# Performance work log

Hardware: AMD Instinct MI355X
Metric: run time of the kernel (lower is better)

The kernel has to match this reference:

```python
import jax, jax.numpy as jnp
import numpy as np

D = 768      # d_model == d_patch (16*16*3)
DFF = 3072
NH = 12
DH = D // NH  # 64
P = 16
IMG = 224
HP = IMG // P  # 14
NP = HP * HP   # 196
L = NP + 1     # 197 with CLS
NL = 12        # layers (weights SHARED across layers, per original code)
NC = 1000


def _pos_enc(length, d):
    # Faithful to PositionalEncoding: even dims sin with exponent i, odd dims cos with exponent i-1
    pos = jnp.arange(length, dtype=jnp.float32)[:, None]          # [L,1]
    dim = jnp.arange(d)
    i = jnp.where(dim % 2 == 0, dim, (dim // 2) * 2).astype(jnp.float32)
    ang = pos / jnp.power(10000.0, i / d)                          # [L,D]
    return jnp.where(dim % 2 == 0, jnp.sin(ang), jnp.cos(ang))


def _ln(x, g, b, eps=1e-5):
    m = x.mean(-1, keepdims=True)
    v = x.var(-1, keepdims=True)
    return (x - m) / jnp.sqrt(v + eps) * g + b


def setup_inputs() -> dict:
    key = jax.random.key(0)
    ks = jax.random.split(key, 12)
    s = 0.02
    n = lambda k, shp: jax.random.normal(k, shp, jnp.float32) * s
    return {
        "x": jax.random.normal(ks[0], (32, 3, IMG, IMG), jnp.float32),
        "w_proj": n(ks[1], (D, D)), "b_proj": jnp.zeros((D,), jnp.float32),
        "cls_emb": jnp.zeros((1, 1, D), jnp.float32),
        "ln1_g": jnp.ones((D,), jnp.float32), "ln1_b": jnp.zeros((D,), jnp.float32),
        "w_qkv": n(ks[2], (3 * D, D)), "b_qkv": jnp.zeros((3 * D,), jnp.float32),
        "w_o": n(ks[3], (D, D)), "b_o": jnp.zeros((D,), jnp.float32),
        "ln2_g": jnp.ones((D,), jnp.float32), "ln2_b": jnp.zeros((D,), jnp.float32),
        "w_fc1": n(ks[4], (DFF, D)), "b_fc1": jnp.zeros((DFF,), jnp.float32),
        "w_fc2": n(ks[5], (D, DFF)), "b_fc2": jnp.zeros((D,), jnp.float32),
        "lnf_g": jnp.ones((D,), jnp.float32), "lnf_b": jnp.zeros((D,), jnp.float32),
        "w_h": n(ks[6], (D, D)), "b_h": jnp.zeros((D,), jnp.float32),
        "w_c": n(ks[7], (NC, D)), "b_c": jnp.zeros((NC,), jnp.float32),
    }


def reference(x, w_proj, b_proj, cls_emb, ln1_g, ln1_b, w_qkv, b_qkv, w_o, b_o,
              ln2_g, ln2_b, w_fc1, b_fc1, w_fc2, b_fc2, lnf_g, lnf_b,
              w_h, b_h, w_c, b_c):
    b = x.shape[0]
    # convert_to_patch: unfold -> channel-major patch features [b, NP, 3*P*P]
    patches = x.reshape(b, 3, HP, P, HP, P).transpose(0, 2, 4, 1, 3, 5).reshape(b, NP, 3 * P * P)
    emb = patches @ w_proj.T + b_proj                              # [b,NP,D]
    cls = jnp.broadcast_to(cls_emb, (b, 1, D))
    h = jnp.concatenate([cls, emb], axis=1) + _pos_enc(L, D)[None]  # [b,L,D]

    inv_sqrt_dk = 1.0 / jnp.sqrt(jnp.float32(DH))
    for _ in range(NL):  # SAME weights every layer (faithful to nn.Sequential of one object)
        y = _ln(h, ln1_g, ln1_b)
        qkv = y @ w_qkv.T + b_qkv                                   # [b,L,3D]
        # faithful non-standard head split: view(b,l,3*DH,NH).transpose -> [b,NH,L,3*DH]
        qkv = qkv.reshape(b, L, 3 * DH, NH).transpose(0, 3, 1, 2)
        q, k, v = jnp.split(qkv, 3, axis=-1)                        # each [b,NH,L,DH]
        attn = jax.nn.softmax(jnp.einsum('bhld,bhmd->bhlm', q, k) * inv_sqrt_dk, axis=-1)
        o = jnp.einsum('bhlm,bhmd->bhld', attn, v)                  # [b,NH,L,DH]
        o = o.transpose(0, 2, 1, 3).reshape(b, L, D)
        h = h + (o @ w_o.T + b_o)
        y = _ln(h, ln2_g, ln2_b)
        f = jax.nn.gelu(y @ w_fc1.T + b_fc1, approximate=False) @ w_fc2.T + b_fc2
        h = h + f

    rep = _ln(h[:, 0], lnf_g, lnf_b)                                # [b,D]
    hid = jnp.tanh(rep @ w_h.T + b_h)                               # is_pretrain=True
    return hid @ w_c.T + b_c                                        # [b,NC]
```

## Files before the change

kernel.cpp:

```cpp
#include <hip/hip_runtime.h>
#include <hip/hip_bf16.h>


typedef __bf16 bf16;
typedef __bf16 bf16x8 __attribute__((ext_vector_type(8)));
typedef __bf16 bf16x4 __attribute__((ext_vector_type(4)));
typedef float  f32x4  __attribute__((ext_vector_type(4)));

typedef __attribute__((address_space(1))) const unsigned int gu32;
typedef __attribute__((address_space(3))) unsigned int lu32;

static __device__ __forceinline__ f32x4 mfma_bf16(bf16x8 a, bf16x8 b, f32x4 c) {
  return __builtin_amdgcn_mfma_f32_16x16x32_bf16(a, b, c, 0, 0, 0);
}
static __device__ __forceinline__ void gll16(const bf16* g, bf16* l) {
  __builtin_amdgcn_global_load_lds((gu32*)g, (lu32*)l, 16, 0, 0);
}


__global__ __launch_bounds__(256) void f2b_k(const float* __restrict__ a, bf16* __restrict__ o, int n) {
  int i = blockIdx.x * 256 + threadIdx.x;
  if (i < n) o[i] = (bf16)a[i];
}

__global__ __launch_bounds__(256) void posenc_k(float* __restrict__ pos) {
  int l = blockIdx.x;
  for (int d = threadIdx.x; d < 768; d += 256) {
    int ieff = d & ~1;
    float ang = (float)l * expf(-(float)ieff * (9.210340371976184f / 768.0f));
    pos[l * 768 + d] = (d & 1) ? cosf(ang) : sinf(ang);
  }
}

__global__ __launch_bounds__(256) void patchify_k(const float* __restrict__ x, bf16* __restrict__ p) {
  int idx = blockIdx.x * 256 + threadIdx.x;
  int t = idx / 768, col = idx - t * 768;
  int b = t / 196, pp = t - b * 196;
  int ph = pp / 14, pw = pp - ph * 14;
  int c = col >> 8, r = col & 255, i = r >> 4, j = r & 15;
  p[idx] = (bf16)x[((b * 3 + c) * 224 + ph * 16 + i) * 224 + pw * 16 + j];
}

__global__ __launch_bounds__(256) void combine_k(float* __restrict__ h, const float* __restrict__ pos,
                                                 const float* __restrict__ cls) {
  int idx = blockIdx.x * 256 + threadIdx.x;
  int t = idx / 768, d = idx - t * 768;
  int l = t % 197;
  float p = pos[l * 768 + d];
  if (l == 0) h[idx] = cls[d] + p;
  else        h[idx] += p;
}

template<int PAD>
__global__ __launch_bounds__(256) void ln4_k(const float* __restrict__ x, const float* __restrict__ g,
                                             const float* __restrict__ bb, bf16* __restrict__ y,
                                             int nrows, int instride) {
  const int wave = threadIdx.x >> 6, lane = threadIdx.x & 63;
  const int row = blockIdx.x * 4 + wave;
  if (row >= nrows) return;
  const float4* x4 = (const float4*)(x + (size_t)row * instride);
  float4 v0 = x4[lane], v1 = x4[lane + 64], v2 = x4[lane + 128];
  float s  = v0.x + v0.y + v0.z + v0.w + v1.x + v1.y + v1.z + v1.w + v2.x + v2.y + v2.z + v2.w;
  float s2 = v0.x*v0.x + v0.y*v0.y + v0.z*v0.z + v0.w*v0.w
           + v1.x*v1.x + v1.y*v1.y + v1.z*v1.z + v1.w*v1.w
           + v2.x*v2.x + v2.y*v2.y + v2.z*v2.z + v2.w*v2.w;
  #pragma unroll
  for (int o = 1; o < 64; o <<= 1) { s += __shfl_xor(s, o); s2 += __shfl_xor(s2, o); }
  float m = s * (1.0f / 768.0f);
  float inv = rsqrtf(s2 * (1.0f / 768.0f) - m * m + 1e-5f);
  int orow = row;
  if (PAD) { int bq = row / 197; orow = row + bq * 3; }
  bf16* yr = y + (size_t)orow * 768;
  const float4* g4 = (const float4*)g;
  const float4* b4 = (const float4*)bb;
  #pragma unroll
  for (int i = 0; i < 3; ++i) {
    int idx = lane + i * 64;
    float4 vv = (i == 0) ? v0 : (i == 1) ? v1 : v2;
    float4 gv = g4[idx], bv = b4[idx];
    bf16x4 o;
    o[0] = (bf16)((vv.x - m) * inv * gv.x + bv.x);
    o[1] = (bf16)((vv.y - m) * inv * gv.y + bv.y);
    o[2] = (bf16)((vv.z - m) * inv * gv.z + bv.z);
    o[3] = (bf16)((vv.w - m) * inv * gv.w + bv.w);
    *(bf16x4*)(yr + idx * 4) = o;
  }
}

template<int BN, int EPI>
__global__ __launch_bounds__(256) void gemm2(
    const bf16* __restrict__ A, const bf16* __restrict__ B,
    int M, int N, int K, int ldc, const float* __restrict__ bias,
    float* __restrict__ outF, bf16* __restrict__ outB)
{
  constexpr int WN = (BN == 128) ? 64 : 32;
  constexpr int NI = WN / 16;
  constexpr int NB = BN / 32;
  __shared__ alignas(16) bf16 As[2][128 * 64];
  __shared__ alignas(16) bf16 Bs[2][BN * 64];
  const int tid = threadIdx.x;
  const int lane = tid & 63, wave = tid >> 6;
  const int wr = wave >> 1, wc = wave & 1;
  const int lrow = lane & 15, lgrp = lane >> 4;
  const int row0 = blockIdx.x * 128, col0 = blockIdx.y * BN;

  f32x4 acc[4][NI] = {};
  const bf16* Agb = A + (size_t)row0 * K;
  const bf16* Bgb = B + (size_t)col0 * K;
  const int srow = lane >> 3, schunk = lane & 7;
  const int nk = K >> 6;

  #pragma unroll
  for (int i = 0; i < 4; ++i) {
    int rr = (wave * 4 + i) * 8 + srow;
    int g = schunk ^ (rr & 7);
    gll16(Agb + (size_t)rr * K + g * 8, As[0] + (wave * 4 + i) * 512);
  }
  #pragma unroll
  for (int i = 0; i < NB; ++i) {
    int rr = (wave * NB + i) * 8 + srow;
    int g = schunk ^ (rr & 7);
    gll16(Bgb + (size_t)rr * K + g * 8, Bs[0] + (wave * NB + i) * 512);
  }
  __syncthreads();

  int cur = 0;
  for (int kt = 0; kt < nk; ++kt) {
    if (kt + 1 < nk) {
      const bf16* Ag = Agb + (kt + 1) * 64;
      const bf16* Bg = Bgb + (kt + 1) * 64;
      bf16* Ad = As[cur ^ 1]; bf16* Bd = Bs[cur ^ 1];
      #pragma unroll
      for (int i = 0; i < 4; ++i) {
        int rr = (wave * 4 + i) * 8 + srow;
        int g = schunk ^ (rr & 7);
        gll16(Ag + (size_t)rr * K + g * 8, Ad + (wave * 4 + i) * 512);
      }
      #pragma unroll
      for (int i = 0; i < NB; ++i) {
        int rr = (wave * NB + i) * 8 + srow;
        int g = schunk ^ (rr & 7);
        gll16(Bg + (size_t)rr * K + g * 8, Bd + (wave * NB + i) * 512);
      }
    }
    const bf16* Ac = As[cur]; const bf16* Bc = Bs[cur];
    #pragma unroll
    for (int kk = 0; kk < 2; ++kk) {
      bf16x8 af[4], bfr[NI];
      #pragma unroll
      for (int mi = 0; mi < 4; ++mi) {
        int r = wr * 64 + mi * 16 + lrow;
        af[mi] = *(const bf16x8*)(Ac + r * 64 + (((kk * 4 + lgrp) ^ (r & 7)) << 3));
      }
      #pragma unroll
      for (int ni = 0; ni < NI; ++ni) {
        int r = wc * WN + ni * 16 + lrow;
        bfr[ni] = *(const bf16x8*)(Bc + r * 64 + (((kk * 4 + lgrp) ^ (r & 7)) << 3));
      }
      __builtin_amdgcn_s_setprio(1);
      #pragma unroll
      for (int mi = 0; mi < 4; ++mi)
        #pragma unroll
        for (int ni = 0; ni < NI; ++ni)
          acc[mi][ni] = mfma_bf16(af[mi], bfr[ni], acc[mi][ni]);
      __builtin_amdgcn_s_setprio(0);
    }
    __syncthreads();
    cur ^= 1;
  }

  #pragma unroll
  for (int ni = 0; ni < NI; ++ni) {
    const int col = col0 + wc * WN + ni * 16 + lrow;
    float bs = 0.0f;
    if (EPI != 1) {
      if (EPI == 5) bs = (col < N) ? bias[col] : 0.0f;
      else          bs = bias[col];
    }
    #pragma unroll
    for (int mi = 0; mi < 4; ++mi) {
      const int rbase = row0 + wr * 64 + mi * 16 + (lgrp << 2);
      #pragma unroll
      for (int j = 0; j < 4; ++j) {
        const int t = rbase + j;
        if (EPI == 1) {
          float val = acc[mi][ni][j] + bias[t];
          if (t < 768) val *= 0.125f;
          outB[(size_t)t * ldc + col] = (bf16)val;
        } else {
          if (t >= M) continue;
          float val = acc[mi][ni][j] + bs;
          if (EPI == 0) {
            int b = t / 196, p = t - b * 196;
            outF[((size_t)(b * 197 + 1 + p)) * 768 + col] = val;
          } else if (EPI == 2) {
            outF[(size_t)t * 768 + col] += val;
          } else if (EPI == 3) {
            outB[(size_t)t * 3072 + col] = (bf16)(0.5f * val * (1.0f + erff(val * 0.70710678118654752f)));
          } else if (EPI == 4) {
            outB[(size_t)t * 768 + col] = (bf16)tanhf(val);
          } else {
            if (col < N) outF[(size_t)t * ldc + col] = val;
          }
        }
      }
    }
  }
}

__global__ __launch_bounds__(512) void attn_k(const bf16* __restrict__ Ct, bf16* __restrict__ O) {
  __shared__ alignas(16) bf16 Ks[208 * 64];
  __shared__ alignas(16) bf16 Qs[208 * 64];
  __shared__ alignas(16) bf16 Vs[64 * 232];
  __shared__ alignas(16) bf16 Ps[8][16 * 232];
  const int bh = blockIdx.x;
  const int b = bh / 12, hh = bh - b * 12;
  const int tid = threadIdx.x, lane = tid & 63, wave = tid >> 6;
  const int lrow = lane & 15, lgrp = lane >> 4;
  const size_t tc0 = (size_t)b * 200;

  for (int task = tid; task < 1600; task += 512) {
    int d = task / 25, lc = task - d * 25;
    int l0 = lc * 8;
    const size_t cb = tc0 + l0;
    bf16x8 qv = *(const bf16x8*)(Ct + ((size_t)(d * 12 + hh)) * 6400 + cb);
    bf16x8 kv = *(const bf16x8*)(Ct + ((size_t)(768 + d * 12 + hh)) * 6400 + cb);
    bf16x8 vv = *(const bf16x8*)(Ct + ((size_t)(1536 + d * 12 + hh)) * 6400 + cb);
    #pragma unroll
    for (int e = 0; e < 8; ++e) {
      int l = l0 + e;
      int sw = ((((d >> 3) ^ (l & 7)) << 3) | (d & 7));
      Ks[l * 64 + sw] = kv[e];
      Qs[l * 64 + sw] = qv[e];
    }
    *(bf16x8*)(Vs + d * 232 + l0) = vv;
  }
  for (int q = tid; q < 64 * 35; q += 512) {
    int d = q / 35, c = 197 + (q - d * 35);
    Vs[d * 232 + c] = (bf16)0.0f;
  }
  __syncthreads();

  for (int rt = wave; rt < 13; rt += 8) {
    const int r = rt * 16 + lrow;
    bf16x8 a0 = *(const bf16x8*)(Qs + r * 64 + ((lgrp ^ (r & 7)) << 3));
    bf16x8 a1 = *(const bf16x8*)(Qs + r * 64 + (((4 + lgrp) ^ (r & 7)) << 3));
    f32x4 sacc[13];
    #pragma unroll
    for (int ct = 0; ct < 13; ++ct) {
      const int kr = ct * 16 + lrow;
      bf16x8 b0 = *(const bf16x8*)(Ks + kr * 64 + ((lgrp ^ (kr & 7)) << 3));
      bf16x8 b1 = *(const bf16x8*)(Ks + kr * 64 + (((4 + lgrp) ^ (kr & 7)) << 3));
      f32x4 s = {};
      s = mfma_bf16(a0, b0, s);
      s = mfma_bf16(a1, b1, s);
      sacc[ct] = s;
    }
    bf16* Pw = Ps[wave];
    float inv4[4];
    #pragma unroll
    for (int j = 0; j < 4; ++j) {
      const int prow = (lgrp << 2) + j;
      float mx = -3.0e38f;
      #pragma unroll
      for (int ct = 0; ct < 13; ++ct) {
        int c = ct * 16 + lrow;
        if (c < 197) mx = fmaxf(mx, sacc[ct][j]);
      }
      #pragma unroll
      for (int o = 1; o < 16; o <<= 1) mx = fmaxf(mx, __shfl_xor(mx, o));
      float sum = 0.0f;
      #pragma unroll
      for (int ct = 0; ct < 13; ++ct) {
        int c = ct * 16 + lrow;
        float p = (c < 197) ? __expf(sacc[ct][j] - mx) : 0.0f;
        sum += p;
        Pw[prow * 232 + c] = (bf16)p;
      }
      #pragma unroll
      for (int o = 1; o < 16; o <<= 1) sum += __shfl_xor(sum, o);
      inv4[j] = 1.0f / sum;
      Pw[prow * 232 + 208 + lrow] = (bf16)0.0f;
    }
    f32x4 oacc[4] = {};
    #pragma unroll
    for (int mc = 0; mc < 7; ++mc) {
      bf16x8 pa = *(const bf16x8*)(Pw + lrow * 232 + mc * 32 + (lgrp << 3));
      #pragma unroll
      for (int n2 = 0; n2 < 4; ++n2) {
        bf16x8 vb = *(const bf16x8*)(Vs + (n2 * 16 + lrow) * 232 + mc * 32 + (lgrp << 3));
        oacc[n2] = mfma_bf16(pa, vb, oacc[n2]);
      }
    }
    #pragma unroll
    for (int n2 = 0; n2 < 4; ++n2) {
      const int d = n2 * 16 + lrow;
      #pragma unroll
      for (int j = 0; j < 4; ++j) {
        const int qrow = rt * 16 + (lgrp << 2) + j;
        if (qrow < 197)
          O[((size_t)b * 197 + qrow) * 768 + hh * 64 + d] = (bf16)(oacc[n2][j] * inv4[j]);
      }
    }
  }
}


extern "C" void kernel_launch(void* const* d_in, const int* in_sizes, int n_in,
                              void* d_out, int out_size, void* d_ws, size_t ws_size,
                              hipStream_t stream) {
  const float* x      = (const float*)d_in[0];
  const float* w_proj = (const float*)d_in[1];
  const float* b_proj = (const float*)d_in[2];
  const float* cls    = (const float*)d_in[3];
  const float* ln1g   = (const float*)d_in[4];
  const float* ln1b   = (const float*)d_in[5];
  const float* w_qkv  = (const float*)d_in[6];
  const float* b_qkv  = (const float*)d_in[7];
  const float* w_o    = (const float*)d_in[8];
  const float* b_o    = (const float*)d_in[9];
  const float* ln2g   = (const float*)d_in[10];
  const float* ln2b   = (const float*)d_in[11];
  const float* w_fc1  = (const float*)d_in[12];
  const float* b_fc1  = (const float*)d_in[13];
  const float* w_fc2  = (const float*)d_in[14];
  const float* b_fc2  = (const float*)d_in[15];
  const float* lnfg   = (const float*)d_in[16];
  const float* lnfb   = (const float*)d_in[17];
  const float* w_h    = (const float*)d_in[18];
  const float* b_h    = (const float*)d_in[19];
  const float* w_c    = (const float*)d_in[20];
  const float* b_c    = (const float*)d_in[21];
  float* out = (float*)d_out;

  uint8_t* ws = (uint8_t*)d_ws;
  size_t off = 0;
  auto alloc = [&](size_t bytes) -> void* {
    void* p = ws + off; off += (bytes + 255) & ~(size_t)255; return p;
  };
  float* h    = (float*)alloc(6400ull * 768 * 4);
  bf16*  ybf  = (bf16*) alloc(6400ull * 768 * 2);
  bf16*  ct   = (bf16*) alloc(2304ull * 6400 * 2);
  bf16*  ob   = (bf16*) alloc(6400ull * 768 * 2);
  bf16*  f1   = (bf16*) alloc(6400ull * 3072 * 2);
  float* pos  = (float*)alloc(197ull * 768 * 4);
  bf16* wprojB = (bf16*)alloc(768ull * 768 * 2);
  bf16* wqkvB  = (bf16*)alloc(2304ull * 768 * 2);
  bf16* woB    = (bf16*)alloc(768ull * 768 * 2);
  bf16* wfc1B  = (bf16*)alloc(3072ull * 768 * 2);
  bf16* wfc2B  = (bf16*)alloc(768ull * 3072 * 2);
  bf16* whB    = (bf16*)alloc(768ull * 768 * 2);
  bf16* wcB    = (bf16*)alloc(1024ull * 768 * 2);
  bf16* repB   = (bf16*)alloc(128ull * 768 * 2);
  bf16* hidB   = (bf16*)alloc(128ull * 768 * 2);
  bf16* patches = f1;

  f2b_k<<<(768 * 768 + 255) / 256, 256, 0, stream>>>(w_proj, wprojB, 768 * 768);
  f2b_k<<<(2304 * 768 + 255) / 256, 256, 0, stream>>>(w_qkv, wqkvB, 2304 * 768);
  f2b_k<<<(768 * 768 + 255) / 256, 256, 0, stream>>>(w_o, woB, 768 * 768);
  f2b_k<<<(3072 * 768 + 255) / 256, 256, 0, stream>>>(w_fc1, wfc1B, 3072 * 768);
  f2b_k<<<(768 * 3072 + 255) / 256, 256, 0, stream>>>(w_fc2, wfc2B, 768 * 3072);
  f2b_k<<<(768 * 768 + 255) / 256, 256, 0, stream>>>(w_h, whB, 768 * 768);
  f2b_k<<<(1000 * 768 + 255) / 256, 256, 0, stream>>>(w_c, wcB, 1000 * 768);
  posenc_k<<<197, 256, 0, stream>>>(pos);
  patchify_k<<<6272 * 768 / 256, 256, 0, stream>>>(x, patches);
  gemm2<64, 0><<<dim3(49, 12), 256, 0, stream>>>(patches, wprojB, 6272, 768, 768, 768, b_proj, h, nullptr);
  combine_k<<<6304 * 768 / 256, 256, 0, stream>>>(h, pos, cls);

  for (int layer = 0; layer < 12; ++layer) {
    ln4_k<1><<<1576, 256, 0, stream>>>(h, ln1g, ln1b, ybf, 6304, 768);
    gemm2<128, 1><<<dim3(18, 50), 256, 0, stream>>>(wqkvB, ybf, 2304, 6400, 768, 6400, b_qkv, nullptr, ct);
    attn_k<<<384, 512, 0, stream>>>(ct, ob);
    gemm2<64, 2><<<dim3(50, 12), 256, 0, stream>>>(ob, woB, 6304, 768, 768, 768, b_o, h, nullptr);
    ln4_k<0><<<1576, 256, 0, stream>>>(h, ln2g, ln2b, ybf, 6304, 768);
    gemm2<128, 3><<<dim3(50, 24), 256, 0, stream>>>(ybf, wfc1B, 6304, 3072, 768, 3072, b_fc1, nullptr, f1);
    gemm2<64, 2><<<dim3(50, 12), 256, 0, stream>>>(f1, wfc2B, 6304, 768, 3072, 768, b_fc2, h, nullptr);
  }

  ln4_k<0><<<8, 256, 0, stream>>>(h, lnfg, lnfb, repB, 32, 197 * 768);
  gemm2<64, 4><<<dim3(1, 12), 256, 0, stream>>>(repB, whB, 32, 768, 768, 768, b_h, nullptr, hidB);
  gemm2<64, 5><<<dim3(1, 16), 256, 0, stream>>>(hidB, wcB, 32, 1000, 768, 1000, b_c, out, nullptr);
}
```

Measured before the change: 2.962 ms.

## Remap GEMM blocks per XCD, single-buffer big tiles, fuse posenc into projection

The GEMM grid becomes 1D, and the block index is remapped so that consecutive tiles land on the same XCD, which should improve L2 reuse of the shared A/B panels on the multi-die GPU. The large-tile GEMMs (QKV, FC1) switch to a single LDS buffer with a sync-load-compute-sync loop, cutting LDS use to raise occupancy at the cost of losing load/compute overlap. The positional-encoding add moves into the patch-projection epilogue, and a tiny kernel writes only the CLS rows, removing a full-tensor pass.

Result: no change. 2.954 ms (-0.3%).

```diff
diff --git a/kernel.cpp b/kernel.cpp
--- a/kernel.cpp
+++ b/kernel.cpp
@@ -41,14 +41,11 @@
   p[idx] = (bf16)x[((b * 3 + c) * 224 + ph * 16 + i) * 224 + pw * 16 + j];
 }
 
-__global__ __launch_bounds__(256) void combine_k(float* __restrict__ h, const float* __restrict__ pos,
-                                                 const float* __restrict__ cls) {
-  int idx = blockIdx.x * 256 + threadIdx.x;
-  int t = idx / 768, d = idx - t * 768;
-  int l = t % 197;
-  float p = pos[l * 768 + d];
-  if (l == 0) h[idx] = cls[d] + p;
-  else        h[idx] += p;
+__global__ __launch_bounds__(256) void cls_k(float* __restrict__ h, const float* __restrict__ pos,
+                                             const float* __restrict__ cls) {
+  int b = blockIdx.x;
+  for (int d = threadIdx.x; d < 768; d += 256)
+    h[((size_t)b * 197) * 768 + d] = cls[d] + pos[d];
 }
 
 template<int PAD>
@@ -87,22 +84,30 @@
   }
 }
 
-template<int BN, int EPI>
+template<int BN, int EPI, bool DBUF>
 __global__ __launch_bounds__(256) void gemm2(
     const bf16* __restrict__ A, const bf16* __restrict__ B,
-    int M, int N, int K, int ldc, const float* __restrict__ bias,
+    int M, int N, int K, int ldc, int gx, const float* __restrict__ bias,
+    const float* __restrict__ posw,
     float* __restrict__ outF, bf16* __restrict__ outB)
 {
   constexpr int WN = (BN == 128) ? 64 : 32;
   constexpr int NI = WN / 16;
   constexpr int NB = BN / 32;
-  __shared__ alignas(16) bf16 As[2][128 * 64];
-  __shared__ alignas(16) bf16 Bs[2][BN * 64];
+  constexpr int NBUF = DBUF ? 2 : 1;
+  __shared__ alignas(16) bf16 As[NBUF][128 * 64];
+  __shared__ alignas(16) bf16 Bs[NBUF][BN * 64];
   const int tid = threadIdx.x;
   const int lane = tid & 63, wave = tid >> 6;
   const int wr = wave >> 1, wc = wave & 1;
   const int lrow = lane & 15, lgrp = lane >> 4;
-  const int row0 = blockIdx.x * 128, col0 = blockIdx.y * BN;
+
+  const int nwg = gridDim.x, bid0 = blockIdx.x;
+  const int xcd = bid0 & 7, loc = bid0 >> 3;
+  const int q = nwg >> 3, r = nwg & 7;
+  const int nb = (xcd < r ? xcd * (q + 1) : r * (q + 1) + (xcd - r) * q) + loc;
+  const int bx = nb % gx, by = nb / gx;
+  const int row0 = bx * 128, col0 = by * BN;
 
   f32x4 acc[4][NI] = {};
   const bf16* Agb = A + (size_t)row0 * K;
@@ -110,52 +115,35 @@
   const int srow = lane >> 3, schunk = lane & 7;
   const int nk = K >> 6;
 
-  #pragma unroll
-  for (int i = 0; i < 4; ++i) {
-    int rr = (wave * 4 + i) * 8 + srow;
-    int g = schunk ^ (rr & 7);
-    gll16(Agb + (size_t)rr * K + g * 8, As[0] + (wave * 4 + i) * 512);
-  }
-  #pragma unroll
-  for (int i = 0; i < NB; ++i) {
-    int rr = (wave * NB + i) * 8 + srow;
-    int g = schunk ^ (rr & 7);
-    gll16(Bgb + (size_t)rr * K + g * 8, Bs[0] + (wave * NB + i) * 512);
-  }
-  __syncthreads();
-
-  int cur = 0;
-  for (int kt = 0; kt < nk; ++kt) {
-    if (kt + 1 < nk) {
-      const bf16* Ag = Agb + (kt + 1) * 64;
-      const bf16* Bg = Bgb + (kt + 1) * 64;
-      bf16* Ad = As[cur ^ 1]; bf16* Bd = Bs[cur ^ 1];
-      #pragma unroll
-      for (int i = 0; i < 4; ++i) {
-        int rr = (wave * 4 + i) * 8 + srow;
-        int g = schunk ^ (rr & 7);
-        gll16(Ag + (size_t)rr * K + g * 8, Ad + (wave * 4 + i) * 512);
-      }
-      #pragma unroll
-      for (int i = 0; i < NB; ++i) {
-        int rr = (wave * NB + i) * 8 + srow;
-        int g = schunk ^ (rr & 7);
-        gll16(Bg + (size_t)rr * K + g * 8, Bd + (wave * NB + i) * 512);
-      }
-    }
-    const bf16* Ac = As[cur]; const bf16* Bc = Bs[cur];
+  auto stageA = [&](const bf16* Ag, bf16* Ad) {
+    #pragma unroll
+    for (int i = 0; i < 4; ++i) {
+      int rr = (wave * 4 + i) * 8 + srow;
+      int g = schunk ^ (rr & 7);
+      gll16(Ag + (size_t)rr * K + g * 8, Ad + (wave * 4 + i) * 512);
+    }
+  };
+  auto stageB = [&](const bf16* Bg, bf16* Bd) {
+    #pragma unroll
+    for (int i = 0; i < NB; ++i) {
+      int rr = (wave * NB + i) * 8 + srow;
+      int g = schunk ^ (rr & 7);
+      gll16(Bg + (size_t)rr * K + g * 8, Bd + (wave * NB + i) * 512);
+    }
+  };
+  auto compute = [&](const bf16* Ac, const bf16* Bc) {
     #pragma unroll
     for (int kk = 0; kk < 2; ++kk) {
       bf16x8 af[4], bfr[NI];
       #pragma unroll
       for (int mi = 0; mi < 4; ++mi) {
-        int r = wr * 64 + mi * 16 + lrow;
-        af[mi] = *(const bf16x8*)(Ac + r * 64 + (((kk * 4 + lgrp) ^ (r & 7)) << 3));
+        int rrr = wr * 64 + mi * 16 + lrow;
+        af[mi] = *(const bf16x8*)(Ac + rrr * 64 + (((kk * 4 + lgrp) ^ (rrr & 7)) << 3));
       }
       #pragma unroll
       for (int ni = 0; ni < NI; ++ni) {
-        int r = wc * WN + ni * 16 + lrow;
-        bfr[ni] = *(const bf16x8*)(Bc + r * 64 + (((kk * 4 + lgrp) ^ (r & 7)) << 3));
+        int rrr = wc * WN + ni * 16 + lrow;
+        bfr[ni] = *(const bf16x8*)(Bc + rrr * 64 + (((kk * 4 + lgrp) ^ (rrr & 7)) << 3));
       }
       __builtin_amdgcn_s_setprio(1);
       #pragma unroll
@@ -165,8 +153,28 @@
           acc[mi][ni] = mfma_bf16(af[mi], bfr[ni], acc[mi][ni]);
       __builtin_amdgcn_s_setprio(0);
     }
+  };
+
+  if constexpr (DBUF) {
+    stageA(Agb, As[0]); stageB(Bgb, Bs[0]);
     __syncthreads();
-    cur ^= 1;
+    int cur = 0;
+    for (int kt = 0; kt < nk; ++kt) {
+      if (kt + 1 < nk) {
+        stageA(Agb + (kt + 1) * 64, As[cur ^ 1]);
+        stageB(Bgb + (kt + 1) * 64, Bs[cur ^ 1]);
+      }
+      compute(As[cur], Bs[cur]);
+      __syncthreads();
+      cur ^= 1;
+    }
+  } else {
+    for (int kt = 0; kt < nk; ++kt) {
+      stageA(Agb + kt * 64, As[0]); stageB(Bgb + kt * 64, Bs[0]);
+      __syncthreads();
+      compute(As[0], Bs[0]);
+      __syncthreads();
+    }
   }
 
   #pragma unroll
@@ -192,7 +200,7 @@
           float val = acc[mi][ni][j] + bs;
           if (EPI == 0) {
             int b = t / 196, p = t - b * 196;
-            outF[((size_t)(b * 197 + 1 + p)) * 768 + col] = val;
+            outF[((size_t)(b * 197 + 1 + p)) * 768 + col] = val + posw[(size_t)(1 + p) * 768 + col];
           } else if (EPI == 2) {
             outF[(size_t)t * 768 + col] += val;
           } else if (EPI == 3) {
@@ -364,20 +372,27 @@
   f2b_k<<<(1000 * 768 + 255) / 256, 256, 0, stream>>>(w_c, wcB, 1000 * 768);
   posenc_k<<<197, 256, 0, stream>>>(pos);
   patchify_k<<<6272 * 768 / 256, 256, 0, stream>>>(x, patches);
-  gemm2<64, 0><<<dim3(49, 12), 256, 0, stream>>>(patches, wprojB, 6272, 768, 768, 768, b_proj, h, nullptr);
-  combine_k<<<6304 * 768 / 256, 256, 0, stream>>>(h, pos, cls);
+  gemm2<64, 0, true><<<49 * 12, 256, 0, stream>>>(patches, wprojB, 6272, 768, 768, 768, 49,
+                                                  b_proj, pos, h, nullptr);
+  cls_k<<<32, 256, 0, stream>>>(h, pos, cls);
 
   for (int layer = 0; layer < 12; ++layer) {
     ln4_k<1><<<1576, 256, 0, stream>>>(h, ln1g, ln1b, ybf, 6304, 768);
-    gemm2<128, 1><<<dim3(18, 50), 256, 0, stream>>>(wqkvB, ybf, 2304, 6400, 768, 6400, b_qkv, nullptr, ct);
+    gemm2<128, 1, false><<<18 * 50, 256, 0, stream>>>(wqkvB, ybf, 2304, 6400, 768, 6400, 18,
+                                                      b_qkv, nullptr, nullptr, ct);
     attn_k<<<384, 512, 0, stream>>>(ct, ob);
-    gemm2<64, 2><<<dim3(50, 12), 256, 0, stream>>>(ob, woB, 6304, 768, 768, 768, b_o, h, nullptr);
+    gemm2<64, 2, true><<<50 * 12, 256, 0, stream>>>(ob, woB, 6304, 768, 768, 768, 50,
+                                                    b_o, nullptr, h, nullptr);
     ln4_k<0><<<1576, 256, 0, stream>>>(h, ln2g, ln2b, ybf, 6304, 768);
-    gemm2<128, 3><<<dim3(50, 24), 256, 0, stream>>>(ybf, wfc1B, 6304, 3072, 768, 3072, b_fc1, nullptr, f1);
-    gemm2<64, 2><<<dim3(50, 12), 256, 0, stream>>>(f1, wfc2B, 6304, 768, 3072, 768, b_fc2, h, nullptr);
+    gemm2<128, 3, false><<<50 * 24, 256, 0, stream>>>(ybf, wfc1B, 6304, 3072, 768, 3072, 50,
+                                                      b_fc1, nullptr, nullptr, f1);
+    gemm2<64, 2, true><<<50 * 12, 256, 0, stream>>>(f1, wfc2B, 6304, 768, 3072, 768, 50,
+                                                    b_fc2, nullptr, h, nullptr);
   }
 
   ln4_k<0><<<8, 256, 0, stream>>>(h, lnfg, lnfb, repB, 32, 197 * 768);
-  gemm2<64, 4><<<dim3(1, 12), 256, 0, stream>>>(repB, whB, 32, 768, 768, 768, b_h, nullptr, hidB);
-  gemm2<64, 5><<<dim3(1, 16), 256, 0, stream>>>(hidB, wcB, 32, 1000, 768, 1000, b_c, out, nullptr);
-}
+  gemm2<64, 4, true><<<1 * 12, 256, 0, stream>>>(repB, whB, 32, 768, 768, 768, 1,
+                                                 b_h, nullptr, nullptr, hidB);
+  gemm2<64, 5, true><<<1 * 16, 256, 0, stream>>>(hidB, wcB, 32, 1000, 768, 1000, 1,
+                                                 b_c, nullptr, out, nullptr);
+}
```
